# Kernel tuning notes

Measured on AMD Instinct MI355X. Metric: run time of the kernel, lower is better.

## Reference

```python
import jax, jax.numpy as jnp
import numpy as np

B, T, C, H = 4, 2048, 1024, 16
D = C // H  # head_dim = 64

def setup_inputs() -> dict:
    key = jax.random.key(0)
    k1, k2, k3 = jax.random.split(key, 3)
    x = jax.random.normal(k1, (B, T, C), dtype=jnp.float32)
    W_attn = jax.random.normal(k2, (C, 3 * C), dtype=jnp.float32) * (C ** -0.5)
    b_attn = jnp.zeros((3 * C,), dtype=jnp.float32)
    W_proj = jax.random.normal(k3, (C, C), dtype=jnp.float32) * (C ** -0.5)
    b_proj = jnp.zeros((C,), dtype=jnp.float32)
    return {"x": x, "W_attn": W_attn, "b_attn": b_attn, "W_proj": W_proj, "b_proj": b_proj}

def reference(x, W_attn, b_attn, W_proj, b_proj):
    Bc, Tc, Cc = x.shape
    qkv = x @ W_attn + b_attn                       # [B,T,3C]
    q, k, v = jnp.split(qkv, 3, axis=-1)
    q = q.reshape(Bc, Tc, H, D).transpose(0, 2, 1, 3)  # [B,H,T,D]
    k = k.reshape(Bc, Tc, H, D).transpose(0, 2, 1, 3)
    v = v.reshape(Bc, Tc, H, D).transpose(0, 2, 1, 3)
    scores = jnp.einsum('bhqd,bhkd->bhqk', q, k) / jnp.sqrt(jnp.float32(D))
    causal = jnp.tril(jnp.ones((Tc, Tc), dtype=bool))
    scores = jnp.where(causal[None, None, :, :], scores, jnp.float32(-jnp.inf))
    wei = jax.nn.softmax(scores, axis=-1)           # dropout=0 -> identity
    out = jnp.einsum('bhqk,bhkd->bhqd', wei, v)     # [B,H,T,D]
    out = out.transpose(0, 2, 1, 3).reshape(Bc, Tc, Cc)
    return out @ W_proj + b_proj
```

## Files before the change

### kernel.cpp

```cpp
#include <hip/hip_runtime.h>
#include <cstdint>
#include <cstddef>

#define Bsz   4
#define Tsz   2048
#define Csz   1024
#define Hn    16
#define Dh    64
#define Mrows 8192
#define KD    1024

#define NEG_BIG (-1.0e30f)
#define SCL2  0.18033688011112042f

typedef unsigned short u16;
typedef __bf16  bf16x8 __attribute__((ext_vector_type(8)));
typedef __bf16  bf16x2 __attribute__((ext_vector_type(2)));
typedef float   f32x4  __attribute__((ext_vector_type(4)));
typedef unsigned int u32x4 __attribute__((ext_vector_type(4)));

__device__ __forceinline__ u16 f2bf(float f) {
  union { float f; unsigned int i; } v; v.f = f;
  unsigned int u = v.i;
  return (u16)((u + 0x7fffu + ((u >> 16) & 1u)) >> 16);
}
__device__ __forceinline__ unsigned int pack2bf(float a, float b) {
#if __has_builtin(__builtin_amdgcn_cvt_pk_bf16_f32)
  union { bf16x2 h; unsigned int u; } cv;
  cv.h = __builtin_amdgcn_cvt_pk_bf16_f32(a, b);
  return cv.u;
#else
  return (unsigned int)f2bf(a) | ((unsigned int)f2bf(b) << 16);
#endif
}
__device__ __forceinline__ unsigned int pack2bf_trunc(float lo, float hi) {
  return __builtin_amdgcn_perm(__builtin_bit_cast(unsigned int, hi),
                               __builtin_bit_cast(unsigned int, lo),
                               0x07060302u);
}
__device__ __forceinline__ float fast_exp2(float x) {
#if __has_builtin(__builtin_amdgcn_exp2f)
  return __builtin_amdgcn_exp2f(x);
#else
  return exp2f(x);
#endif
}

__global__ __launch_bounds__(256)
void cvt_f32_bf16(const float* __restrict__ in, u16* __restrict__ out, int n4) {
  const int i = blockIdx.x * 256 + threadIdx.x;
  if (i >= n4) return;
  const float4 v = ((const float4*)in)[i];
  uint2 o;
  o.x = pack2bf(v.x, v.y);
  o.y = pack2bf(v.z, v.w);
  ((uint2*)out)[i] = o;
}

__global__ __launch_bounds__(256)
void transpose_f32_bf16(const float* __restrict__ in, u16* __restrict__ out,
                        int rows, int cols) {
  __shared__ u16 tile[64][65];
  const int tc = blockIdx.x * 64, tr = blockIdx.y * 64;
  const int x = threadIdx.x & 63, y0 = threadIdx.x >> 6;
#pragma unroll
  for (int yy = 0; yy < 64; yy += 4) {
    int r = yy + y0;
    tile[r][x] = f2bf(in[(size_t)(tr + r) * cols + tc + x]);
  }
  __syncthreads();
#pragma unroll
  for (int yy = 0; yy < 64; yy += 4) {
    int r = yy + y0;
    out[(size_t)(tc + r) * rows + tr + x] = tile[x][r];
  }
}

template<int MODE>
__global__ __launch_bounds__(256)
void gemm_bt(const u16* __restrict__ A, const u16* __restrict__ BT,
             const float* __restrict__ bias, u16* __restrict__ o0,
             u16* __restrict__ o1, u16* __restrict__ o2,
             float* __restrict__ fout, int N) {
  __shared__ u16 lsA[128 * 32];
  __shared__ u16 lsB[128 * 32];
  const int tid  = threadIdx.x;
  const int lane = tid & 63;
  const int wid  = tid >> 6;
  const int wm   = wid & 1, wn = wid >> 1;
  const int quad = lane >> 4, l15 = lane & 15;
  const int m0 = blockIdx.y * 128, n0 = blockIdx.x * 128;

  f32x4 acc[4][4];
#pragma unroll
  for (int i = 0; i < 4; ++i)
#pragma unroll
    for (int j = 0; j < 4; ++j) acc[i][j] = (f32x4){0.f, 0.f, 0.f, 0.f};

#if __has_builtin(__builtin_amdgcn_global_load_lds)
  const int srow = lane >> 2, schunk = lane & 3;
  const u16* gA = A  + (size_t)(m0 + wid * 32 + srow) * KD + schunk * 8;
  const u16* gB = BT + (size_t)(n0 + wid * 32 + srow) * KD + schunk * 8;
  u16* lA0 = &lsA[(wid * 32) * 32];
  u16* lB0 = &lsB[(wid * 32) * 32];
#endif

  for (int kk = 0; kk < KD; kk += 32) {
#if __has_builtin(__builtin_amdgcn_global_load_lds)
#pragma unroll
    for (int i = 0; i < 2; ++i) {
      __builtin_amdgcn_global_load_lds(
          (const __attribute__((address_space(1))) void*)(gA + (size_t)i * 16 * KD + kk),
          (__attribute__((address_space(3))) void*)(lA0 + i * 16 * 32), 16, 0, 0);
      __builtin_amdgcn_global_load_lds(
          (const __attribute__((address_space(1))) void*)(gB + (size_t)i * 16 * KD + kk),
          (__attribute__((address_space(3))) void*)(lB0 + i * 16 * 32), 16, 0, 0);
    }
#else
#pragma unroll
    for (int cc = 0; cc < 2; ++cc) {
      int c = tid + cc * 256;
      int row = c >> 2, ch = c & 3;
      *(uint4*)&lsA[row * 32 + ch * 8] =
          *(const uint4*)&A[(size_t)(m0 + row) * KD + kk + ch * 8];
      *(uint4*)&lsB[row * 32 + ch * 8] =
          *(const uint4*)&BT[(size_t)(n0 + row) * KD + kk + ch * 8];
    }
#endif
    __syncthreads();
    bf16x8 af[4], bfv[4];
#pragma unroll
    for (int i = 0; i < 4; ++i)
      af[i] = *(const bf16x8*)&lsA[(wm * 64 + i * 16 + l15) * 32 + quad * 8];
#pragma unroll
    for (int j = 0; j < 4; ++j)
      bfv[j] = *(const bf16x8*)&lsB[(wn * 64 + j * 16 + l15) * 32 + quad * 8];
#pragma unroll
    for (int i = 0; i < 4; ++i)
#pragma unroll
      for (int j = 0; j < 4; ++j)
        acc[i][j] = __builtin_amdgcn_mfma_f32_16x16x32_bf16(af[i], bfv[j],
                                                            acc[i][j], 0, 0, 0);
    __syncthreads();
  }

#pragma unroll
  for (int i = 0; i < 4; ++i) {
#pragma unroll
    for (int j = 0; j < 4; ++j) {
      const int colb = n0 + wn * 64 + j * 16 + l15;
      const float bv = bias[colb];
      float vals[4];
#pragma unroll
      for (int r = 0; r < 4; ++r) vals[r] = acc[i][j][r] + bv;
      const int row0 = m0 + wm * 64 + i * 16 + quad * 4;
      if (MODE == 0) {
        const int b = row0 >> 11, t0 = row0 & (Tsz - 1);
        const int region = colb >> 10;
        const int nc = colb & (Csz - 1);
        const int h = nc >> 6, d = nc & 63;
        if (region == 2) {
          uint2 st;
          st.x = pack2bf(vals[0], vals[1]);
          st.y = pack2bf(vals[2], vals[3]);
          *(uint2*)&o2[((size_t)((b << 4) + h) * Dh + d) * Tsz + t0] = st;
        } else {
          u16* dst = (region == 0) ? o0 : o1;
          const float qs = (region == 0) ? SCL2 : 1.0f;
#pragma unroll
          for (int r = 0; r < 4; ++r)
            dst[(size_t)(((b << 4) + h) * Tsz + t0 + r) * Dh + d] =
                f2bf(vals[r] * qs);
        }
      } else {
#pragma unroll
        for (int r = 0; r < 4; ++r)
          fout[(size_t)(row0 + r) * N + colb] = vals[r];
      }
    }
  }
}

__global__ __launch_bounds__(256)
void attn_fused(const u16* __restrict__ qb, const u16* __restrict__ kbuf,
                const u16* __restrict__ vT, u16* __restrict__ outp) {
  __shared__ u16 Kl[2][64 * 64];
  __shared__ u16 Vt[2][64 * 64];
  const int tid = threadIdx.x, lane = tid & 63, w = tid >> 6;
  const int quad = lane >> 4, l15 = lane & 15;
  const int cswz = (l15 & 7) << 3;
  const int bh = blockIdx.x;
  const int b = bh >> 4, h = bh & 15;
  const u16* Q   = qb   + (size_t)bh * Tsz * Dh;
  const u16* Kg  = kbuf + (size_t)bh * Tsz * Dh;
  const u16* VTg = vT   + (size_t)bh * Dh * Tsz;

  const int srow   = lane >> 3;
  const int schunk = ((lane & 7) ^ srow) << 3;
  const u16* gK0 = Kg  + (size_t)(w * 16 + srow) * Dh  + schunk;
  const u16* gV0 = VTg + (size_t)(w * 16 + srow) * Tsz + schunk;

#if __has_builtin(__builtin_amdgcn_global_load_lds)
#define STAGE(jj, bb) do {                                                     \
    const size_t kb_ = (size_t)(jj) * 64;                                      \
    _Pragma("unroll")                                                          \
    for (int i_ = 0; i_ < 2; ++i_) {                                           \
      __builtin_amdgcn_global_load_lds(                                        \
        (const __attribute__((address_space(1))) void*)(gK0 + (kb_ + (size_t)i_ * 8) * Dh), \
        (__attribute__((address_space(3))) void*)(&Kl[bb][(w * 16 + i_ * 8) * 64]), 16, 0, 0); \
      __builtin_amdgcn_global_load_lds(                                        \
        (const __attribute__((address_space(1))) void*)(gV0 + (size_t)(i_ * 8) * Tsz + kb_), \
        (__attribute__((address_space(3))) void*)(&Vt[bb][(w * 16 + i_ * 8) * 64]), 16, 0, 0); \
    }                                                                          \
  } while (0)
#else
#define STAGE(jj, bb) do {                                                     \
    const int kb_ = (jj) * 64;                                                 \
    _Pragma("unroll")                                                          \
    for (int cc_ = 0; cc_ < 2; ++cc_) {                                        \
      const int c_ = tid + cc_ * 256;                                          \
      const int rr_ = c_ >> 3, off_ = c_ & 7;                                  \
      const int dc_ = (off_ ^ (rr_ & 7)) << 3;                                 \
      *(uint4*)&Kl[bb][rr_ * 64 + dc_] =                                       \
          *(const uint4*)&Kg[(size_t)(kb_ + rr_) * Dh + off_ * 8];             \
      *(uint4*)&Vt[bb][rr_ * 64 + dc_] =                                       \
          *(const uint4*)&VTg[(size_t)rr_ * Tsz + kb_ + off_ * 8];             \
    }                                                                          \
  } while (0)
#endif

  for (int ph = 0; ph < 2; ++ph) {
    const int jq = ph ? (int)blockIdx.y : 31 - (int)blockIdx.y;

    const int qrow = jq * 64 + w * 16 + l15;
    const bf16x8 bq0 = *(const bf16x8*)&Q[(size_t)qrow * Dh + quad * 8];
    const bf16x8 bq1 = *(const bf16x8*)&Q[(size_t)qrow * Dh + 32 + quad * 8];

    f32x4 O[4];
#pragma unroll
    for (int nb = 0; nb < 4; ++nb) O[nb] = (f32x4){0.f, 0.f, 0.f, 0.f};
    float l_i = 0.f;

    STAGE(0, 0);
    __syncthreads();

    for (int j = 0; j <= jq; ++j) {
      const int cur = j & 1;
      if (j < jq) STAGE(j + 1, cur ^ 1);

      const int kb = j * 64;
      const bool diag = (j == jq);
      const int tmax = diag ? (w + 1) : 4;
      const u16* KT = Kl[cur];
      const u16* VL = Vt[cur];

      f32x4 S[4];
#pragma unroll
      for (int t = 0; t < 4; ++t) S[t] = (f32x4){0.f, 0.f, 0.f, 0.f};
#pragma unroll
      for (int t = 0; t < 4; ++t) {
        if (t < tmax) {
          bf16x8 ak = *(const bf16x8*)&KT[(t * 16 + l15) * 64 + ((quad * 8) ^ cswz)];
          S[t] = __builtin_amdgcn_mfma_f32_16x16x32_bf16(ak, bq0, S[t], 0, 0, 0);
          ak = *(const bf16x8*)&KT[(t * 16 + l15) * 64 + ((quad * 8 + 32) ^ cswz)];
          S[t] = __builtin_amdgcn_mfma_f32_16x16x32_bf16(ak, bq1, S[t], 0, 0, 0);
        }
      }

      float p[4][4];
      if (diag) {
#pragma unroll
        for (int t = 0; t < 4; ++t) {
          const int key0 = kb + t * 16 + quad * 4;
#pragma unroll
          for (int r = 0; r < 4; ++r) {
            const float sv =
                (t < tmax && key0 + r <= qrow) ? S[t][r] : NEG_BIG;
            p[t][r] = fast_exp2(sv);
            l_i += p[t][r];
          }
        }
      } else {
#pragma unroll
        for (int t = 0; t < 4; ++t)
#pragma unroll
          for (int r = 0; r < 4; ++r) {
            p[t][r] = fast_exp2(S[t][r]);
            l_i += p[t][r];
          }
      }

      u32x4 pu;
      pu[0] = pack2bf_trunc(p[0][0], p[0][1]);
      pu[1] = pack2bf_trunc(p[0][2], p[0][3]);
      pu[2] = pack2bf_trunc(p[1][0], p[1][1]);
      pu[3] = pack2bf_trunc(p[1][2], p[1][3]);
      bf16x8 pb = __builtin_bit_cast(bf16x8, pu);
#pragma unroll
      for (int nb = 0; nb < 4; ++nb) {
        const uint2 a0 = *(const uint2*)&VL[(nb * 16 + l15) * 64 + ((quad * 4) ^ cswz)];
        const uint2 a1 = *(const uint2*)&VL[(nb * 16 + l15) * 64 + ((quad * 4 + 16) ^ cswz)];
        const u32x4 au = {a0.x, a0.y, a1.x, a1.y};
        O[nb] = __builtin_amdgcn_mfma_f32_16x16x32_bf16(
            __builtin_bit_cast(bf16x8, au), pb, O[nb], 0, 0, 0);
      }
      if (tmax > 2) {
        pu[0] = pack2bf_trunc(p[2][0], p[2][1]);
        pu[1] = pack2bf_trunc(p[2][2], p[2][3]);
        pu[2] = pack2bf_trunc(p[3][0], p[3][1]);
        pu[3] = pack2bf_trunc(p[3][2], p[3][3]);
        pb = __builtin_bit_cast(bf16x8, pu);
#pragma unroll
        for (int nb = 0; nb < 4; ++nb) {
          const uint2 a0 = *(const uint2*)&VL[(nb * 16 + l15) * 64 + ((quad * 4 + 32) ^ cswz)];
          const uint2 a1 = *(const uint2*)&VL[(nb * 16 + l15) * 64 + ((quad * 4 + 48) ^ cswz)];
          const u32x4 au = {a0.x, a0.y, a1.x, a1.y};
          O[nb] = __builtin_amdgcn_mfma_f32_16x16x32_bf16(
              __builtin_bit_cast(bf16x8, au), pb, O[nb], 0, 0, 0);
        }
      }
      __syncthreads();
    }

    float lt = l_i + __shfl_xor(l_i, 16, 64);
    lt += __shfl_xor(lt, 32, 64);
    const float inv = 1.0f / lt;
#pragma unroll
    for (int nb = 0; nb < 4; ++nb) {
      uint2 st;
      st.x = pack2bf(O[nb][0] * inv, O[nb][1] * inv);
      st.y = pack2bf(O[nb][2] * inv, O[nb][3] * inv);
      *(uint2*)&outp[(size_t)(b * Tsz + qrow) * Csz + h * Dh + nb * 16 + quad * 4] = st;
    }
  }
#undef STAGE
}

extern "C" void kernel_launch(void* const* d_in, const int* in_sizes, int n_in,
                              void* d_out, int out_size, void* d_ws, size_t ws_size,
                              hipStream_t stream) {
  const float* x      = (const float*)d_in[0];
  const float* W_attn = (const float*)d_in[1];
  const float* b_attn = (const float*)d_in[2];
  const float* W_proj = (const float*)d_in[3];
  const float* b_proj = (const float*)d_in[4];
  float* out = (float*)d_out;

  u16* ws   = (u16*)d_ws;
  u16* xbf  = ws;
  u16* qbuf = xbf  + (size_t)Mrows * Csz;
  u16* kbuf = qbuf + (size_t)Mrows * Csz;
  u16* vbuf = kbuf + (size_t)Mrows * Csz;
  u16* aout = vbuf + (size_t)Mrows * Csz;
  u16* WTa  = aout + (size_t)Mrows * Csz;
  u16* WTp  = WTa  + (size_t)Csz * 3 * Csz;

  cvt_f32_bf16<<<(Mrows * Csz / 4 + 255) / 256, 256, 0, stream>>>(
      x, xbf, Mrows * Csz / 4);
  transpose_f32_bf16<<<dim3(3 * Csz / 64, Csz / 64), 256, 0, stream>>>(
      W_attn, WTa, Csz, 3 * Csz);
  transpose_f32_bf16<<<dim3(Csz / 64, Csz / 64), 256, 0, stream>>>(
      W_proj, WTp, Csz, Csz);
  gemm_bt<0><<<dim3(3 * Csz / 128, Mrows / 128), 256, 0, stream>>>(
      xbf, WTa, b_attn, qbuf, kbuf, vbuf, nullptr, 3 * Csz);
  attn_fused<<<dim3(Bsz * Hn, Tsz / 128), 256, 0, stream>>>(
      qbuf, kbuf, vbuf, aout);
  gemm_bt<1><<<dim3(Csz / 128, Mrows / 128), 256, 0, stream>>>(
      aout, WTp, b_proj, nullptr, nullptr, nullptr, out, Csz);
}
```

Before: 256.5 us.

## Double-buffer GEMM K-loop, merge prep kernels, refine attention sync and priority

The three prep kernels (x conversion and two weight transposes) become one launch. The GEMM moves to a K-step of 64 with double-buffered, XOR-swizzled LDS tiles and explicit vmcnt waits, so the next tile's global-to-LDS load overlaps the current MFMAs. In attention, __syncthreads is replaced with explicit vmcnt waits plus raw barriers, and s_setprio is raised around the MFMA blocks. This cuts launch overhead and exposed load latency, but doubles GEMM LDS use and relies on exact waitcnt counts being correct.

```diff
diff --git a/kernel.cpp b/kernel.cpp
--- a/kernel.cpp
+++ b/kernel.cpp
@@ -18,6 +18,10 @@
 typedef __bf16  bf16x2 __attribute__((ext_vector_type(2)));
 typedef float   f32x4  __attribute__((ext_vector_type(4)));
 typedef unsigned int u32x4 __attribute__((ext_vector_type(4)));
+
+#define BARRIER() do { asm volatile("" ::: "memory");                          \
+                       __builtin_amdgcn_s_barrier();                           \
+                       asm volatile("" ::: "memory"); } while (0)
 
 __device__ __forceinline__ u16 f2bf(float f) {
   union { float f; unsigned int i; } v; v.f = f;
@@ -46,33 +50,46 @@
 #endif
 }
 
+#define CVT_BLKS  (Mrows * Csz / 4 / 256)
+#define TRA_BLKS  (48 * 16)
+#define TRP_BLKS  (16 * 16)
+
 __global__ __launch_bounds__(256)
-void cvt_f32_bf16(const float* __restrict__ in, u16* __restrict__ out, int n4) {
-  const int i = blockIdx.x * 256 + threadIdx.x;
-  if (i >= n4) return;
-  const float4 v = ((const float4*)in)[i];
-  uint2 o;
-  o.x = pack2bf(v.x, v.y);
-  o.y = pack2bf(v.z, v.w);
-  ((uint2*)out)[i] = o;
-}
-
-__global__ __launch_bounds__(256)
-void transpose_f32_bf16(const float* __restrict__ in, u16* __restrict__ out,
-                        int rows, int cols) {
+void prep(const float* __restrict__ x, u16* __restrict__ xbf,
+          const float* __restrict__ Wa, u16* __restrict__ WTa,
+          const float* __restrict__ Wp, u16* __restrict__ WTp) {
   __shared__ u16 tile[64][65];
-  const int tc = blockIdx.x * 64, tr = blockIdx.y * 64;
-  const int x = threadIdx.x & 63, y0 = threadIdx.x >> 6;
+  int bid = blockIdx.x;
+  const int tid = threadIdx.x;
+  if (bid < CVT_BLKS) {
+    const int i = bid * 256 + tid;
+    const float4 v = ((const float4*)x)[i];
+    uint2 o;
+    o.x = pack2bf(v.x, v.y);
+    o.y = pack2bf(v.z, v.w);
+    ((uint2*)xbf)[i] = o;
+    return;
+  }
+  bid -= CVT_BLKS;
+  const float* in; u16* out; int cols, bx, by;
+  if (bid < TRA_BLKS) {
+    in = Wa; out = WTa; cols = 3 * Csz; bx = bid % 48; by = bid / 48;
+  } else {
+    bid -= TRA_BLKS;
+    in = Wp; out = WTp; cols = Csz; bx = bid & 15; by = bid >> 4;
+  }
+  const int tc = bx * 64, tr = by * 64;
+  const int xx = tid & 63, y0 = tid >> 6;
 #pragma unroll
   for (int yy = 0; yy < 64; yy += 4) {
     int r = yy + y0;
-    tile[r][x] = f2bf(in[(size_t)(tr + r) * cols + tc + x]);
+    tile[r][xx] = f2bf(in[(size_t)(tr + r) * cols + tc + xx]);
   }
   __syncthreads();
 #pragma unroll
   for (int yy = 0; yy < 64; yy += 4) {
     int r = yy + y0;
-    out[(size_t)(tc + r) * rows + tr + x] = tile[x][r];
+    out[(size_t)(tc + r) * Csz + tr + xx] = tile[xx][r];
   }
 }
 
@@ -82,13 +99,14 @@
              const float* __restrict__ bias, u16* __restrict__ o0,
              u16* __restrict__ o1, u16* __restrict__ o2,
              float* __restrict__ fout, int N) {
-  __shared__ u16 lsA[128 * 32];
-  __shared__ u16 lsB[128 * 32];
+  __shared__ u16 lsA[2][128 * 64];
+  __shared__ u16 lsB[2][128 * 64];
   const int tid  = threadIdx.x;
   const int lane = tid & 63;
   const int wid  = tid >> 6;
   const int wm   = wid & 1, wn = wid >> 1;
   const int quad = lane >> 4, l15 = lane & 15;
+  const int rswz = l15 & 7;
   const int m0 = blockIdx.y * 128, n0 = blockIdx.x * 128;
 
   f32x4 acc[4][4];
@@ -97,52 +115,74 @@
 #pragma unroll
     for (int j = 0; j < 4; ++j) acc[i][j] = (f32x4){0.f, 0.f, 0.f, 0.f};
 
-#if __has_builtin(__builtin_amdgcn_global_load_lds)
-  const int srow = lane >> 2, schunk = lane & 3;
+  const int srow   = lane >> 3;
+  const int schunk = (lane & 7) ^ srow;
   const u16* gA = A  + (size_t)(m0 + wid * 32 + srow) * KD + schunk * 8;
   const u16* gB = BT + (size_t)(n0 + wid * 32 + srow) * KD + schunk * 8;
-  u16* lA0 = &lsA[(wid * 32) * 32];
-  u16* lB0 = &lsB[(wid * 32) * 32];
+
+#if __has_builtin(__builtin_amdgcn_global_load_lds)
+#define GSTAGE(t_, bb_) do {                                                   \
+    _Pragma("unroll")                                                          \
+    for (int i_ = 0; i_ < 4; ++i_) {                                           \
+      __builtin_amdgcn_global_load_lds(                                        \
+        (const __attribute__((address_space(1))) void*)(gA + (size_t)i_ * 8 * KD + (t_) * 64), \
+        (__attribute__((address_space(3))) void*)(&lsA[bb_][(wid * 32 + i_ * 8) * 64]), 16, 0, 0); \
+      __builtin_amdgcn_global_load_lds(                                        \
+        (const __attribute__((address_space(1))) void*)(gB + (size_t)i_ * 8 * KD + (t_) * 64), \
+        (__attribute__((address_space(3))) void*)(&lsB[bb_][(wid * 32 + i_ * 8) * 64]), 16, 0, 0); \
+    }                                                                          \
+  } while (0)
+#else
+#define GSTAGE(t_, bb_) do {                                                   \
+    _Pragma("unroll")                                                          \
+    for (int cc_ = 0; cc_ < 4; ++cc_) {                                        \
+      const int c_ = tid + cc_ * 256;                                          \
+      const int rr_ = c_ >> 3, off_ = c_ & 7;                                  \
+      const int dc_ = (off_ ^ (rr_ & 7)) << 3;                                 \
+      *(uint4*)&lsA[bb_][rr_ * 64 + dc_] =                                     \
+          *(const uint4*)&A[(size_t)(m0 + rr_) * KD + (t_) * 64 + off_ * 8];   \
+      *(uint4*)&lsB[bb_][rr_ * 64 + dc_] =                                     \
+          *(const uint4*)&BT[(size_t)(n0 + rr_) * KD + (t_) * 64 + off_ * 8];  \
+    }                                                                          \
+  } while (0)
 #endif
 
-  for (int kk = 0; kk < KD; kk += 32) {
-#if __has_builtin(__builtin_amdgcn_global_load_lds)
-#pragma unroll
-    for (int i = 0; i < 2; ++i) {
-      __builtin_amdgcn_global_load_lds(
-          (const __attribute__((address_space(1))) void*)(gA + (size_t)i * 16 * KD + kk),
-          (__attribute__((address_space(3))) void*)(lA0 + i * 16 * 32), 16, 0, 0);
-      __builtin_amdgcn_global_load_lds(
-          (const __attribute__((address_space(1))) void*)(gB + (size_t)i * 16 * KD + kk),
-          (__attribute__((address_space(3))) void*)(lB0 + i * 16 * 32), 16, 0, 0);
+  GSTAGE(0, 0);
+  const int KT = KD / 64;
+  for (int t = 0; t < KT; ++t) {
+    const int cur = t & 1;
+    if (t < KT - 1) {
+      GSTAGE(t + 1, cur ^ 1);
+      asm volatile("s_waitcnt vmcnt(8)" ::: "memory");
+    } else {
+      asm volatile("s_waitcnt vmcnt(0)" ::: "memory");
     }
-#else
-#pragma unroll
-    for (int cc = 0; cc < 2; ++cc) {
-      int c = tid + cc * 256;
-      int row = c >> 2, ch = c & 3;
-      *(uint4*)&lsA[row * 32 + ch * 8] =
-          *(const uint4*)&A[(size_t)(m0 + row) * KD + kk + ch * 8];
-      *(uint4*)&lsB[row * 32 + ch * 8] =
-          *(const uint4*)&BT[(size_t)(n0 + row) * KD + kk + ch * 8];
-    }
-#endif
-    __syncthreads();
-    bf16x8 af[4], bfv[4];
-#pragma unroll
-    for (int i = 0; i < 4; ++i)
-      af[i] = *(const bf16x8*)&lsA[(wm * 64 + i * 16 + l15) * 32 + quad * 8];
-#pragma unroll
-    for (int j = 0; j < 4; ++j)
-      bfv[j] = *(const bf16x8*)&lsB[(wn * 64 + j * 16 + l15) * 32 + quad * 8];
-#pragma unroll
-    for (int i = 0; i < 4; ++i)
-#pragma unroll
-      for (int j = 0; j < 4; ++j)
-        acc[i][j] = __builtin_amdgcn_mfma_f32_16x16x32_bf16(af[i], bfv[j],
-                                                            acc[i][j], 0, 0, 0);
-    __syncthreads();
-  }
+    BARRIER();
+
+    bf16x8 af[4][2], bfv[4][2];
+#pragma unroll
+    for (int m = 0; m < 4; ++m)
+#pragma unroll
+      for (int ks = 0; ks < 2; ++ks)
+        af[m][ks] = *(const bf16x8*)
+            &lsA[cur][(wm * 64 + m * 16 + l15) * 64 + (((ks * 4 + quad) ^ rswz) << 3)];
+#pragma unroll
+    for (int n = 0; n < 4; ++n)
+#pragma unroll
+      for (int ks = 0; ks < 2; ++ks)
+        bfv[n][ks] = *(const bf16x8*)
+            &lsB[cur][(wn * 64 + n * 16 + l15) * 64 + (((ks * 4 + quad) ^ rswz) << 3)];
+#pragma unroll
+    for (int m = 0; m < 4; ++m)
+#pragma unroll
+      for (int n = 0; n < 4; ++n)
+#pragma unroll
+        for (int ks = 0; ks < 2; ++ks)
+          acc[m][n] = __builtin_amdgcn_mfma_f32_16x16x32_bf16(
+              af[m][ks], bfv[n][ks], acc[m][n], 0, 0, 0);
+    BARRIER();
+  }
+#undef GSTAGE
 
 #pragma unroll
   for (int i = 0; i < 4; ++i) {
@@ -242,11 +282,16 @@
     float l_i = 0.f;
 
     STAGE(0, 0);
-    __syncthreads();
 
     for (int j = 0; j <= jq; ++j) {
       const int cur = j & 1;
-      if (j < jq) STAGE(j + 1, cur ^ 1);
+      if (j < jq) {
+        STAGE(j + 1, cur ^ 1);
+        asm volatile("s_waitcnt vmcnt(4)" ::: "memory");
+      } else {
+        asm volatile("s_waitcnt vmcnt(0)" ::: "memory");
+      }
+      BARRIER();
 
       const int kb = j * 64;
       const bool diag = (j == jq);
@@ -257,6 +302,7 @@
       f32x4 S[4];
 #pragma unroll
       for (int t = 0; t < 4; ++t) S[t] = (f32x4){0.f, 0.f, 0.f, 0.f};
+      __builtin_amdgcn_s_setprio(1);
 #pragma unroll
       for (int t = 0; t < 4; ++t) {
         if (t < tmax) {
@@ -266,6 +312,7 @@
           S[t] = __builtin_amdgcn_mfma_f32_16x16x32_bf16(ak, bq1, S[t], 0, 0, 0);
         }
       }
+      __builtin_amdgcn_s_setprio(0);
 
       float p[4][4];
       if (diag) {
@@ -296,6 +343,7 @@
       pu[2] = pack2bf_trunc(p[1][0], p[1][1]);
       pu[3] = pack2bf_trunc(p[1][2], p[1][3]);
       bf16x8 pb = __builtin_bit_cast(bf16x8, pu);
+      __builtin_amdgcn_s_setprio(1);
 #pragma unroll
       for (int nb = 0; nb < 4; ++nb) {
         const uint2 a0 = *(const uint2*)&VL[(nb * 16 + l15) * 64 + ((quad * 4) ^ cswz)];
@@ -304,12 +352,14 @@
         O[nb] = __builtin_amdgcn_mfma_f32_16x16x32_bf16(
             __builtin_bit_cast(bf16x8, au), pb, O[nb], 0, 0, 0);
       }
+      __builtin_amdgcn_s_setprio(0);
       if (tmax > 2) {
         pu[0] = pack2bf_trunc(p[2][0], p[2][1]);
         pu[1] = pack2bf_trunc(p[2][2], p[2][3]);
         pu[2] = pack2bf_trunc(p[3][0], p[3][1]);
         pu[3] = pack2bf_trunc(p[3][2], p[3][3]);
         pb = __builtin_bit_cast(bf16x8, pu);
+        __builtin_amdgcn_s_setprio(1);
 #pragma unroll
         for (int nb = 0; nb < 4; ++nb) {
           const uint2 a0 = *(const uint2*)&VL[(nb * 16 + l15) * 64 + ((quad * 4 + 32) ^ cswz)];
@@ -318,8 +368,9 @@
           O[nb] = __builtin_amdgcn_mfma_f32_16x16x32_bf16(
               __builtin_bit_cast(bf16x8, au), pb, O[nb], 0, 0, 0);
         }
-      }
-      __syncthreads();
+        __builtin_amdgcn_s_setprio(0);
+      }
+      BARRIER();
     }
 
     float lt = l_i + __shfl_xor(l_i, 16, 64);
@@ -355,12 +406,8 @@
   u16* WTa  = aout + (size_t)Mrows * Csz;
   u16* WTp  = WTa  + (size_t)Csz * 3 * Csz;
 
-  cvt_f32_bf16<<<(Mrows * Csz / 4 + 255) / 256, 256, 0, stream>>>(
-      x, xbf, Mrows * Csz / 4);
-  transpose_f32_bf16<<<dim3(3 * Csz / 64, Csz / 64), 256, 0, stream>>>(
-      W_attn, WTa, Csz, 3 * Csz);
-  transpose_f32_bf16<<<dim3(Csz / 64, Csz / 64), 256, 0, stream>>>(
-      W_proj, WTp, Csz, Csz);
+  prep<<<CVT_BLKS + TRA_BLKS + TRP_BLKS, 256, 0, stream>>>(
+      x, xbf, W_attn, WTa, W_proj, WTp);
   gemm_bt<0><<<dim3(3 * Csz / 128, Mrows / 128), 256, 0, stream>>>(
       xbf, WTa, b_attn, qbuf, kbuf, vbuf, nullptr, 3 * Csz);
   attn_fused<<<dim3(Bsz * Hn, Tsz / 128), 256, 0, stream>>>(
```

Result: faster. 247.1 us (-3.6%).
